# Kernel optimization log

Measured on AMD Instinct MI355X. Metric: run time of the kernel, lower is better.

## Reference

```python
import jax, jax.numpy as jnp
import numpy as np

N_NODES = 100000


def gcn_conv(x, edge_index, W, b):
    """PyG GCNConv: add self-loops, symmetric deg^{-1/2} A deg^{-1/2} aggregation.

    x: [N, Fin], edge_index: [2, E] int (row 0 = src, row 1 = dst).
    Transform first (Fin -> Fout), then gather-normalize-scatter at Fout.
    """
    n = x.shape[0]
    loops = jnp.arange(n, dtype=edge_index.dtype)
    src = jnp.concatenate([edge_index[0], loops])
    dst = jnp.concatenate([edge_index[1], loops])
    # in-degree with self-loops (all edge weights = 1)
    deg = jax.ops.segment_sum(jnp.ones_like(dst, dtype=x.dtype), dst, num_segments=n)
    dinv = jax.lax.rsqrt(deg)  # deg >= 1 thanks to self-loops
    norm = dinv[src] * dinv[dst]  # [E+N]
    h = x @ W  # [N, Fout] dense transform before sparse aggregation
    msgs = norm[:, None] * h[src]  # gather + normalize
    out = jax.ops.segment_sum(msgs, dst, num_segments=n)  # scatter-add
    return out + b


def setup_inputs() -> dict:
    key = jax.random.key(0)
    ks = jax.random.split(key, 8)
    N, E, Fin, H, C = N_NODES, 1600000, 256, 64, 11
    x = jax.random.normal(ks[0], (N, Fin), dtype=jnp.float32)
    edge_index = jax.random.randint(ks[1], (2, E), 0, N, dtype=jnp.int64)
    s1 = 1.0 / np.sqrt(Fin)
    s2 = 1.0 / np.sqrt(H)
    W1 = jax.random.uniform(ks[2], (Fin, H), jnp.float32, -s1, s1)
    b1 = jnp.zeros((H,), jnp.float32)
    W2 = jax.random.uniform(ks[3], (H, H), jnp.float32, -s2, s2)
    b2 = jnp.zeros((H,), jnp.float32)
    Wfc = jax.random.uniform(ks[4], (H, C), jnp.float32, -s2, s2)
    bfc = jax.random.uniform(ks[5], (C,), jnp.float32, -s2, s2)
    return {"x": x, "edge_index": edge_index, "W1": W1, "b1": b1,
            "W2": W2, "b2": b2, "Wfc": Wfc, "bfc": bfc}


def reference(x, edge_index, W1, b1, W2, b2, Wfc, bfc):
    h = jax.nn.relu(gcn_conv(x, edge_index, W1, b1))
    h = jax.nn.relu(gcn_conv(h, edge_index, W2, b2))
    return h @ Wfc + bfc  # [N, 11]
```

## Files before the change

kernel.cpp:

```cpp
#include <hip/hip_runtime.h>
#include <hip/hip_fp16.h>

#define NFEAT 64
#define CE 8192
#define EBUF 4608

typedef _Float16 half8 __attribute__((ext_vector_type(8)));
typedef float f32x4 __attribute__((ext_vector_type(4)));

__device__ __forceinline__ __half2 bch(unsigned int u) {
    return __builtin_bit_cast(__half2, u);
}

__global__ __launch_bounds__(256) void k_prep(
    const float* __restrict__ W1, __half* __restrict__ Wt1,
    const float* __restrict__ W2, __half* __restrict__ Wt2,
    const int* __restrict__ eiDst, int* __restrict__ hist, int E, int nbkt)
{
    __shared__ int hb[512];
    int bid = blockIdx.x, tid = threadIdx.x;
    if (bid < 64) {
        int idx = bid * 256 + tid;
        int n = idx >> 8, k = idx & 255;
        Wt1[idx] = __float2half(W1[(size_t)k * NFEAT + n]);
    } else if (bid < 80) {
        int idx = (bid - 64) * 256 + tid;
        int n = idx >> 6, k = idx & 63;
        Wt2[idx] = __float2half(W2[(size_t)k * NFEAT + n]);
    } else {
        int c = bid - 80;
        int base = c * CE;
        if (base >= E) return;
        for (int i = tid; i < nbkt; i += 256) hb[i] = 0;
        __syncthreads();
        int hi = min(base + CE, E);
        for (int e = base + tid; e < hi; e += 256)
            atomicAdd(&hb[eiDst[e] >> 8], 1);
        __syncthreads();
        for (int i = tid; i < nbkt; i += 256)
            hist[(size_t)c * nbkt + i] = hb[i];
    }
}

__global__ __launch_bounds__(256) void k_scanB(int* __restrict__ hist,
                                               int* __restrict__ cntB,
                                               int nchk, int nbkt) {
    __shared__ int hb[256];
    int b = blockIdx.x, tid = threadIdx.x;
    int v = (tid < nchk) ? hist[(size_t)tid * nbkt + b] : 0;
    hb[tid] = v;
    __syncthreads();
    for (int off = 1; off < 256; off <<= 1) {
        int t = (tid >= off) ? hb[tid - off] : 0;
        __syncthreads();
        if (tid >= off) hb[tid] += t;
        __syncthreads();
    }
    if (tid < nchk) hist[(size_t)tid * nbkt + b] = hb[tid] - v;
    if (tid == 255) cntB[b] = hb[255];
}

__global__ __launch_bounds__(256) void k_scatter(
    const int* __restrict__ ei, const int* __restrict__ hist,
    const int* __restrict__ cntB, int2* __restrict__ E2, int E, int nbkt)
{
    __shared__ int2 ebuf[CE];
    __shared__ int lofs[512];
    __shared__ int gbase[512];
    __shared__ int cur[512];
    __shared__ int hb[256];
    int c = blockIdx.x, tid = threadIdx.x;
    int base = c * CE, hi = min(base + CE, E), ne = hi - base;

    for (int i = tid; i < nbkt; i += 256) cur[i] = 0;
    __syncthreads();
    for (int e = base + tid; e < hi; e += 256)
        atomicAdd(&cur[ei[(size_t)E + e] >> 8], 1);
    __syncthreads();

    int i0 = 2 * tid, i1 = 2 * tid + 1;
    int a0 = (i0 < nbkt) ? cur[i0] : 0;
    int a1 = (i1 < nbkt) ? cur[i1] : 0;
    hb[tid] = a0 + a1;
    __syncthreads();
    for (int off = 1; off < 256; off <<= 1) {
        int t = (tid >= off) ? hb[tid - off] : 0;
        __syncthreads();
        if (tid >= off) hb[tid] += t;
        __syncthreads();
    }
    int excl = hb[tid] - (a0 + a1);
    if (i0 < nbkt) lofs[i0] = excl;
    if (i1 < nbkt) lofs[i1] = excl + a0;

    int b0 = (i0 < nbkt) ? cntB[i0] : 0;
    int b1 = (i1 < nbkt) ? cntB[i1] : 0;
    hb[tid] = b0 + b1;
    __syncthreads();
    for (int off = 1; off < 256; off <<= 1) {
        int t = (tid >= off) ? hb[tid - off] : 0;
        __syncthreads();
        if (tid >= off) hb[tid] += t;
        __syncthreads();
    }
    int excl2 = hb[tid] - (b0 + b1);
    if (i0 < nbkt) gbase[i0] = excl2 + hist[(size_t)c * nbkt + i0];
    if (i1 < nbkt) gbase[i1] = excl2 + b0 + hist[(size_t)c * nbkt + i1];

    for (int i = tid; i < nbkt; i += 256) cur[i] = lofs[i];
    __syncthreads();
    for (int e = base + tid; e < hi; e += 256) {
        int s = ei[e];
        int d = ei[(size_t)E + e];
        int p = atomicAdd(&cur[d >> 8], 1);
        ebuf[p] = make_int2(s, d);
    }
    __syncthreads();

    for (int i = tid; i < ne; i += 256) {
        int2 e = ebuf[i];
        int b = e.y >> 8;
        E2[gbase[b] + (i - lofs[b])] = e;
    }
}

__global__ __launch_bounds__(256) void k_csr(
    const int2* __restrict__ E2, const int* __restrict__ cntB,
    int* __restrict__ rowptr, float* __restrict__ dinv, int* __restrict__ col,
    int N, int E, int nbkt)
{
    __shared__ int2 ebuf[EBUF];
    __shared__ int cnt[256];
    __shared__ float dl[256];
    __shared__ int bbL[512];
    __shared__ int hb[256];
    int b = blockIdx.x, tid = threadIdx.x;

    int i0 = 2 * tid, i1 = 2 * tid + 1;
    int a0 = (i0 < nbkt) ? cntB[i0] : 0;
    int a1 = (i1 < nbkt) ? cntB[i1] : 0;
    hb[tid] = a0 + a1;
    __syncthreads();
    for (int off = 1; off < 256; off <<= 1) {
        int t = (tid >= off) ? hb[tid - off] : 0;
        __syncthreads();
        if (tid >= off) hb[tid] += t;
        __syncthreads();
    }
    int excl = hb[tid] - (a0 + a1);
    if (i0 < nbkt) bbL[i0] = excl;
    if (i1 < nbkt) bbL[i1] = excl + a0;
    __syncthreads();

    int e0 = bbL[b];
    int e1 = (b == nbkt - 1) ? E : bbL[b + 1];
    int ne = e1 - e0;
    int nL = min(ne, EBUF);

    cnt[tid] = 0;
    __syncthreads();
    for (int i = tid; i < nL; i += 256) {
        int2 e = E2[e0 + i];
        ebuf[i] = e;
        atomicAdd(&cnt[e.y & 255], 1);
    }
    for (int i = nL + tid; i < ne; i += 256) {
        int2 e = E2[e0 + i];
        atomicAdd(&cnt[e.y & 255], 1);
    }
    __syncthreads();
    int c = cnt[tid];
    dl[tid] = rsqrtf((float)(c + 1));
    for (int off = 1; off < 256; off <<= 1) {
        int t = (tid >= off) ? cnt[tid - off] : 0;
        __syncthreads();
        if (tid >= off) cnt[tid] += t;
        __syncthreads();
    }
    int texcl = cnt[tid] - c;
    int node = b * 256 + tid;
    if (node < N) {
        rowptr[node] = e0 + texcl;
        dinv[node] = dl[tid];
    }
    if (b == 0 && tid == 0) rowptr[N] = E;
    __syncthreads();
    cnt[tid] = texcl;
    __syncthreads();
    for (int i = tid; i < nL; i += 256) {
        int2 e = ebuf[i];
        int p = atomicAdd(&cnt[e.y & 255], 1);
        col[e0 + p] = e.x;
    }
    for (int i = nL + tid; i < ne; i += 256) {
        int2 e = E2[e0 + i];
        int p = atomicAdd(&cnt[e.y & 255], 1);
        col[e0 + p] = e.x;
    }
}

__global__ __launch_bounds__(256) void k_gemm1(
    const float* __restrict__ A, const __half* __restrict__ Wt,
    const float* __restrict__ dinv, __half* __restrict__ H, int M)
{
    const int K = 256;
    int tid = threadIdx.x;
    int w = tid >> 6, lane = tid & 63;
    int q = lane >> 4, n16 = lane & 15;
    int m0 = blockIdx.x * 64;

    int arow = m0 + w * 16 + n16;
    if (arow > M - 1) arow = M - 1;
    const float* ap = A + (size_t)arow * K + q * 8;
    const __half* wp = Wt + (size_t)n16 * K + q * 8;

    f32x4 acc[4];
#pragma unroll
    for (int nt = 0; nt < 4; ++nt) acc[nt] = (f32x4)(0.f);

#pragma unroll
    for (int kt = 0; kt < 8; ++kt) {
        float4 f0 = *(const float4*)(ap + kt * 32);
        float4 f1 = *(const float4*)(ap + kt * 32 + 4);
        float fv[8] = {f0.x, f0.y, f0.z, f0.w, f1.x, f1.y, f1.z, f1.w};
        half8 ahi, alo;
#pragma unroll
        for (int j = 0; j < 8; ++j) {
            _Float16 hi = (_Float16)fv[j];
            ahi[j] = hi;
            alo[j] = (_Float16)(fv[j] - (float)hi);
        }
#pragma unroll
        for (int nt = 0; nt < 4; ++nt) {
            uint4 u = *(const uint4*)(wp + (size_t)(nt * 16) * K + kt * 32);
            half8 b = __builtin_bit_cast(half8, u);
            acc[nt] = __builtin_amdgcn_mfma_f32_16x16x32_f16(ahi, b, acc[nt], 0, 0, 0);
            acc[nt] = __builtin_amdgcn_mfma_f32_16x16x32_f16(alo, b, acc[nt], 0, 0, 0);
        }
    }

#pragma unroll
    for (int reg = 0; reg < 4; ++reg) {
        int row = m0 + w * 16 + q * 4 + reg;
        if (row < M) {
            float di = dinv[row];
#pragma unroll
            for (int nt = 0; nt < 4; ++nt)
                H[(size_t)row * NFEAT + nt * 16 + n16] =
                    __float2half(di * acc[nt][reg]);
        }
    }
}

__global__ __launch_bounds__(256) void k_ag1g2(
    const __half* __restrict__ h, const int* __restrict__ rowptr,
    const int* __restrict__ col, const float* __restrict__ dinv,
    const float* __restrict__ b1, const __half* __restrict__ Wt2,
    __half* __restrict__ H2, int n)
{
    __shared__ float Bs[64][68];
    int tid = threadIdx.x;
    int w = tid >> 6, lane = tid & 63;
    int li = lane & 7, fi = li << 3;
    int slot = (w << 3) | (lane >> 3);

    const __half* hp = h + fi;
    auto ld = [&](int src) { return *(const uint4*)(hp + (size_t)src * NFEAT); };

#pragma unroll
    for (int hf = 0; hf < 2; ++hf) {
        int lr = hf * 32 + slot;
        int r = blockIdx.x * 64 + lr;
        float t0 = 0.f, t1 = 0.f, t2 = 0.f, t3 = 0.f,
              t4 = 0.f, t5 = 0.f, t6 = 0.f, t7 = 0.f;
        if (r < n) {
            float a0 = 0.f, a1 = 0.f, a2 = 0.f, a3 = 0.f,
                  a4 = 0.f, a5 = 0.f, a6 = 0.f, a7 = 0.f;
            auto addu = [&](uint4 u) {
                float2 f0 = __half22float2(bch(u.x));
                float2 f1 = __half22float2(bch(u.y));
                float2 f2 = __half22float2(bch(u.z));
                float2 f3 = __half22float2(bch(u.w));
                a0 += f0.x; a1 += f0.y; a2 += f1.x; a3 += f1.y;
                a4 += f2.x; a5 += f2.y; a6 += f3.x; a7 += f3.y;
            };
            auto p2 = [&](uint4 u0, uint4 u1) {
                uint4 s;
                s.x = __builtin_bit_cast(unsigned int, __hadd2(bch(u0.x), bch(u1.x)));
                s.y = __builtin_bit_cast(unsigned int, __hadd2(bch(u0.y), bch(u1.y)));
                s.z = __builtin_bit_cast(unsigned int, __hadd2(bch(u0.z), bch(u1.z)));
                s.w = __builtin_bit_cast(unsigned int, __hadd2(bch(u0.w), bch(u1.w)));
                addu(s);
            };
            int beg = rowptr[r], end = rowptr[r + 1];
            addu(ld(r));
            int j = beg;
            for (; j + 3 < end; j += 4) {
                uint4 u0 = ld(col[j]);
                uint4 u1 = ld(col[j + 1]);
                uint4 u2 = ld(col[j + 2]);
                uint4 u3 = ld(col[j + 3]);
                p2(u0, u1);
                p2(u2, u3);
            }
            for (; j < end; ++j) addu(ld(col[j]));
            float di = dinv[r];
            t0 = fmaxf(b1[fi + 0] + di * a0, 0.f);
            t1 = fmaxf(b1[fi + 1] + di * a1, 0.f);
            t2 = fmaxf(b1[fi + 2] + di * a2, 0.f);
            t3 = fmaxf(b1[fi + 3] + di * a3, 0.f);
            t4 = fmaxf(b1[fi + 4] + di * a4, 0.f);
            t5 = fmaxf(b1[fi + 5] + di * a5, 0.f);
            t6 = fmaxf(b1[fi + 6] + di * a6, 0.f);
            t7 = fmaxf(b1[fi + 7] + di * a7, 0.f);
        }
        *(float4*)&Bs[lr][fi]     = make_float4(t0, t1, t2, t3);
        *(float4*)&Bs[lr][fi + 4] = make_float4(t4, t5, t6, t7);
    }
    __syncthreads();

    int q = lane >> 4, n16 = lane & 15;
    f32x4 acc[4];
#pragma unroll
    for (int nt = 0; nt < 4; ++nt) acc[nt] = (f32x4)(0.f);
    const __half* wp = Wt2 + (size_t)n16 * 64 + q * 8;

#pragma unroll
    for (int kt = 0; kt < 2; ++kt) {
        const float* ap = &Bs[w * 16 + n16][kt * 32 + q * 8];
        float4 f0 = *(const float4*)ap;
        float4 f1 = *(const float4*)(ap + 4);
        float fv[8] = {f0.x, f0.y, f0.z, f0.w, f1.x, f1.y, f1.z, f1.w};
        half8 ahi, alo;
#pragma unroll
        for (int j = 0; j < 8; ++j) {
            _Float16 hi = (_Float16)fv[j];
            ahi[j] = hi;
            alo[j] = (_Float16)(fv[j] - (float)hi);
        }
#pragma unroll
        for (int nt = 0; nt < 4; ++nt) {
            uint4 u = *(const uint4*)(wp + (size_t)(nt * 16) * 64 + kt * 32);
            half8 b = __builtin_bit_cast(half8, u);
            acc[nt] = __builtin_amdgcn_mfma_f32_16x16x32_f16(ahi, b, acc[nt], 0, 0, 0);
            acc[nt] = __builtin_amdgcn_mfma_f32_16x16x32_f16(alo, b, acc[nt], 0, 0, 0);
        }
    }
#pragma unroll
    for (int reg = 0; reg < 4; ++reg) {
        int row = blockIdx.x * 64 + w * 16 + q * 4 + reg;
        if (row < n) {
            float di = dinv[row];
#pragma unroll
            for (int nt = 0; nt < 4; ++nt)
                H2[(size_t)row * NFEAT + nt * 16 + n16] =
                    __float2half(di * acc[nt][reg]);
        }
    }
}

__global__ __launch_bounds__(256) void k_aggr2(
    const __half* __restrict__ h, const int* __restrict__ rowptr,
    const int* __restrict__ col, const float* __restrict__ dinv,
    const float* __restrict__ bias, const float* __restrict__ Wfc,
    const float* __restrict__ bfc, float* __restrict__ out, int n)
{
    __shared__ float Wl[NFEAT * 11 + 11];
    int tid = threadIdx.x;
    for (int i = tid; i < NFEAT * 11; i += 256) Wl[i] = Wfc[i];
    if (tid < 11) Wl[NFEAT * 11 + tid] = bfc[tid];
    __syncthreads();

    int lane = tid & 63;
    int li = lane & 7;
    int fi = li << 3;
    int r = blockIdx.x * 32 + ((tid >> 6) << 3) + (lane >> 3);
    bool valid = r < n;

    int beg = 0, end = 0;
    if (valid) { beg = rowptr[r]; end = rowptr[r + 1]; }

    const __half* hp = h + fi;
    auto ld = [&](int src) { return *(const uint4*)(hp + (size_t)src * NFEAT); };

    float a0 = 0.f, a1 = 0.f, a2 = 0.f, a3 = 0.f,
          a4 = 0.f, a5 = 0.f, a6 = 0.f, a7 = 0.f;
    auto addu = [&](uint4 u) {
        float2 f0 = __half22float2(bch(u.x));
        float2 f1 = __half22float2(bch(u.y));
        float2 f2 = __half22float2(bch(u.z));
        float2 f3 = __half22float2(bch(u.w));
        a0 += f0.x; a1 += f0.y; a2 += f1.x; a3 += f1.y;
        a4 += f2.x; a5 += f2.y; a6 += f3.x; a7 += f3.y;
    };
    auto p2 = [&](uint4 u0, uint4 u1) {
        uint4 s;
        s.x = __builtin_bit_cast(unsigned int, __hadd2(bch(u0.x), bch(u1.x)));
        s.y = __builtin_bit_cast(unsigned int, __hadd2(bch(u0.y), bch(u1.y)));
        s.z = __builtin_bit_cast(unsigned int, __hadd2(bch(u0.z), bch(u1.z)));
        s.w = __builtin_bit_cast(unsigned int, __hadd2(bch(u0.w), bch(u1.w)));
        addu(s);
    };

    if (valid) addu(ld(r));
    int j = beg;
    for (; j + 3 < end; j += 4) {
        uint4 u0 = ld(col[j]);
        uint4 u1 = ld(col[j + 1]);
        uint4 u2 = ld(col[j + 2]);
        uint4 u3 = ld(col[j + 3]);
        p2(u0, u1);
        p2(u2, u3);
    }
    for (; j < end; ++j) addu(ld(col[j]));

    if (!valid) return;
    float di = dinv[r];
    float t0 = fmaxf(bias[fi + 0] + di * a0, 0.f);
    float t1 = fmaxf(bias[fi + 1] + di * a1, 0.f);
    float t2 = fmaxf(bias[fi + 2] + di * a2, 0.f);
    float t3 = fmaxf(bias[fi + 3] + di * a3, 0.f);
    float t4 = fmaxf(bias[fi + 4] + di * a4, 0.f);
    float t5 = fmaxf(bias[fi + 5] + di * a5, 0.f);
    float t6 = fmaxf(bias[fi + 6] + di * a6, 0.f);
    float t7 = fmaxf(bias[fi + 7] + di * a7, 0.f);

#pragma unroll
    for (int c = 0; c < 11; ++c) {
        const float* wc = &Wl[fi * 11 + c];
        float p = t0 * wc[0] + t1 * wc[11] + t2 * wc[22] + t3 * wc[33]
                + t4 * wc[44] + t5 * wc[55] + t6 * wc[66] + t7 * wc[77];
        p += __shfl_xor(p, 1, 64);
        p += __shfl_xor(p, 2, 64);
        p += __shfl_xor(p, 4, 64);
        if (li == 0) out[(size_t)r * 11 + c] = p + Wl[NFEAT * 11 + c];
    }
}

extern "C" void kernel_launch(void* const* d_in, const int* in_sizes, int n_in,
                              void* d_out, int out_size, void* d_ws, size_t ws_size,
                              hipStream_t stream) {
    const float* x   = (const float*)d_in[0];
    const int*   ei  = (const int*)d_in[1];
    const float* W1  = (const float*)d_in[2];
    const float* b1  = (const float*)d_in[3];
    const float* W2  = (const float*)d_in[4];
    const float* b2  = (const float*)d_in[5];
    const float* Wfc = (const float*)d_in[6];
    const float* bfc = (const float*)d_in[7];
    float* out = (float*)d_out;

    const int Fin = 256;
    int N = in_sizes[0] / Fin;
    int E = in_sizes[1] / 2;

    char* ws = (char*)d_ws;
    size_t off = 0;
    auto alloc = [&](size_t bytes) { void* p = ws + off; off = (off + bytes + 255) & ~(size_t)255; return p; };
    int*    rowptr = (int*)   alloc((size_t)(N + 1) * 4);
    float*  dinv   = (float*) alloc((size_t)N * 4);
    int*    col    = (int*)   alloc((size_t)E * 4);
    __half* Wt1    = (__half*)alloc((size_t)64 * 256 * 2);
    __half* Wt2    = (__half*)alloc((size_t)64 * 64 * 2);
    __half* A      = (__half*)alloc((size_t)N * NFEAT * 2);
    __half* H2     = (__half*)alloc((size_t)N * NFEAT * 2);

    int NBKT = (N + 255) >> 8;
    int NCHK = (E + CE - 1) / CE;

    int2* E2   = (int2*)alloc((size_t)E * 8);
    int*  hist = (int*) alloc((size_t)NCHK * NBKT * 4);
    int*  cntB = (int*) alloc((size_t)NBKT * 4);

    int gb = (N + 63) / 64;
    int gA = (N + 31) / 32;

    k_prep<<<80 + NCHK, 256, 0, stream>>>(W1, Wt1, W2, Wt2, ei + E, hist, E, NBKT);

    k_scanB<<<NBKT, 256, 0, stream>>>(hist, cntB, NCHK, NBKT);
    k_scatter<<<NCHK, 256, 0, stream>>>(ei, hist, cntB, E2, E, NBKT);
    k_csr<<<NBKT, 256, 0, stream>>>(E2, cntB, rowptr, dinv, col, N, E, NBKT);

    k_gemm1<<<gb, 256, 0, stream>>>(x, Wt1, dinv, A, N);

    k_ag1g2<<<gb, 256, 0, stream>>>(A, rowptr, col, dinv, b1, Wt2, H2, N);

    k_aggr2<<<gA, 256, 0, stream>>>(H2, rowptr, col, dinv, b2, Wfc, bfc, out, N);
}
```

Measured before the change: 331.9 us.

## Split GEMM1 into quarters co-scheduled with the CSR build kernels

The first dense transform no longer depends on dinv. Its 64-row tiles are split into four slices and appended as extra blocks to the histogram, scan, scatter and CSR kernels, so the tensor-core GEMM runs alongside the latency-bound graph preprocessing instead of after it. Because the source-side dinv scaling is removed from GEMM1, layer-1 aggregation now loads dinv per neighbor and uses FMA accumulation in fp32 instead of paired fp16 adds, at the cost of extra gathers. It also caches the block's rowptr slice in shared memory, and the layer-2 aggregation loop gains an 8-way unrolled stage.

After: 327.2 us. No clear change (-1.4%).

```diff
diff --git a/kernel.cpp b/kernel.cpp
--- a/kernel.cpp
+++ b/kernel.cpp
@@ -12,41 +12,111 @@
     return __builtin_bit_cast(__half2, u);
 }
 
-__global__ __launch_bounds__(256) void k_prep(
+__device__ __forceinline__ void gemm1_tile(
+    const float* __restrict__ X, const __half* __restrict__ Wt,
+    __half* __restrict__ H, int M, int tileIdx, int tid)
+{
+    const int K = 256;
+    int w = tid >> 6, lane = tid & 63;
+    int q = lane >> 4, n16 = lane & 15;
+    int m0 = tileIdx * 64;
+
+    int arow = m0 + w * 16 + n16;
+    if (arow > M - 1) arow = M - 1;
+    const float* ap = X + (size_t)arow * K + q * 8;
+    const __half* wp = Wt + (size_t)n16 * K + q * 8;
+
+    f32x4 acc[4];
+#pragma unroll
+    for (int nt = 0; nt < 4; ++nt) acc[nt] = (f32x4)(0.f);
+
+#pragma unroll
+    for (int kt = 0; kt < 8; ++kt) {
+        float4 f0 = *(const float4*)(ap + kt * 32);
+        float4 f1 = *(const float4*)(ap + kt * 32 + 4);
+        float fv[8] = {f0.x, f0.y, f0.z, f0.w, f1.x, f1.y, f1.z, f1.w};
+        half8 ahi, alo;
+#pragma unroll
+        for (int j = 0; j < 8; ++j) {
+            _Float16 hi = (_Float16)fv[j];
+            ahi[j] = hi;
+            alo[j] = (_Float16)(fv[j] - (float)hi);
+        }
+#pragma unroll
+        for (int nt = 0; nt < 4; ++nt) {
+            uint4 u = *(const uint4*)(wp + (size_t)(nt * 16) * K + kt * 32);
+            half8 b = __builtin_bit_cast(half8, u);
+            acc[nt] = __builtin_amdgcn_mfma_f32_16x16x32_f16(ahi, b, acc[nt], 0, 0, 0);
+            acc[nt] = __builtin_amdgcn_mfma_f32_16x16x32_f16(alo, b, acc[nt], 0, 0, 0);
+        }
+    }
+
+#pragma unroll
+    for (int reg = 0; reg < 4; ++reg) {
+        int row = m0 + w * 16 + q * 4 + reg;
+        if (row < M) {
+#pragma unroll
+            for (int nt = 0; nt < 4; ++nt)
+                H[(size_t)row * NFEAT + nt * 16 + n16] =
+                    __float2half(acc[nt][reg]);
+        }
+    }
+}
+
+__global__ __launch_bounds__(256) void k_cvtW(
     const float* __restrict__ W1, __half* __restrict__ Wt1,
-    const float* __restrict__ W2, __half* __restrict__ Wt2,
-    const int* __restrict__ eiDst, int* __restrict__ hist, int E, int nbkt)
-{
-    __shared__ int hb[512];
+    const float* __restrict__ W2, __half* __restrict__ Wt2)
+{
     int bid = blockIdx.x, tid = threadIdx.x;
     if (bid < 64) {
         int idx = bid * 256 + tid;
         int n = idx >> 8, k = idx & 255;
         Wt1[idx] = __float2half(W1[(size_t)k * NFEAT + n]);
-    } else if (bid < 80) {
+    } else {
         int idx = (bid - 64) * 256 + tid;
         int n = idx >> 6, k = idx & 63;
         Wt2[idx] = __float2half(W2[(size_t)k * NFEAT + n]);
-    } else {
-        int c = bid - 80;
-        int base = c * CE;
-        if (base >= E) return;
-        for (int i = tid; i < nbkt; i += 256) hb[i] = 0;
-        __syncthreads();
-        int hi = min(base + CE, E);
-        for (int e = base + tid; e < hi; e += 256)
-            atomicAdd(&hb[eiDst[e] >> 8], 1);
-        __syncthreads();
-        for (int i = tid; i < nbkt; i += 256)
-            hist[(size_t)c * nbkt + i] = hb[i];
-    }
-}
-
-__global__ __launch_bounds__(256) void k_scanB(int* __restrict__ hist,
-                                               int* __restrict__ cntB,
-                                               int nchk, int nbkt) {
+    }
+}
+
+__global__ __launch_bounds__(256) void k_hist_g(
+    const int* __restrict__ eiDst, int* __restrict__ hist, int E, int nbkt,
+    const float* __restrict__ X, const __half* __restrict__ Wt1,
+    __half* __restrict__ A, int M, int nsp, int tbase, int ntile)
+{
+    __shared__ int hb[512];
+    int bid = blockIdx.x, tid = threadIdx.x;
+    if (bid >= nsp) {
+        int t = tbase + (bid - nsp);
+        if (t < ntile) gemm1_tile(X, Wt1, A, M, t, tid);
+        return;
+    }
+    int c = bid;
+    int base = c * CE;
+    if (base >= E) return;
+    for (int i = tid; i < nbkt; i += 256) hb[i] = 0;
+    __syncthreads();
+    int hi = min(base + CE, E);
+    for (int e = base + tid; e < hi; e += 256)
+        atomicAdd(&hb[eiDst[e] >> 8], 1);
+    __syncthreads();
+    for (int i = tid; i < nbkt; i += 256)
+        hist[(size_t)c * nbkt + i] = hb[i];
+}
+
+__global__ __launch_bounds__(256) void k_scanB_g(
+    int* __restrict__ hist, int* __restrict__ cntB, int nchk, int nbkt,
+    const float* __restrict__ X, const __half* __restrict__ Wt1,
+    __half* __restrict__ A, int M, int nsp, int tbase, int ntile)
+{
     __shared__ int hb[256];
-    int b = blockIdx.x, tid = threadIdx.x;
+    int bid = blockIdx.x, tid = threadIdx.x;
+    if (bid >= nsp) {
+        int t = tbase + (bid - nsp);
+        if (t < ntile) gemm1_tile(X, Wt1, A, M, t, tid);
+        return;
+    }
+    int b = bid;
     int v = (tid < nchk) ? hist[(size_t)tid * nbkt + b] : 0;
     hb[tid] = v;
     __syncthreads();
@@ -60,16 +130,24 @@
     if (tid == 255) cntB[b] = hb[255];
 }
 
-__global__ __launch_bounds__(256) void k_scatter(
+__global__ __launch_bounds__(256) void k_scatter_g(
     const int* __restrict__ ei, const int* __restrict__ hist,
-    const int* __restrict__ cntB, int2* __restrict__ E2, int E, int nbkt)
+    const int* __restrict__ cntB, int2* __restrict__ E2, int E, int nbkt,
+    const float* __restrict__ X, const __half* __restrict__ Wt1,
+    __half* __restrict__ A, int M, int nsp, int tbase, int ntile)
 {
     __shared__ int2 ebuf[CE];
     __shared__ int lofs[512];
     __shared__ int gbase[512];
     __shared__ int cur[512];
     __shared__ int hb[256];
-    int c = blockIdx.x, tid = threadIdx.x;
+    int bid = blockIdx.x, tid = threadIdx.x;
+    if (bid >= nsp) {
+        int t = tbase + (bid - nsp);
+        if (t < ntile) gemm1_tile(X, Wt1, A, M, t, tid);
+        return;
+    }
+    int c = bid;
     int base = c * CE, hi = min(base + CE, E), ne = hi - base;
 
     for (int i = tid; i < nbkt; i += 256) cur[i] = 0;
@@ -124,17 +202,25 @@
     }
 }
 
-__global__ __launch_bounds__(256) void k_csr(
+__global__ __launch_bounds__(256) void k_csr_g(
     const int2* __restrict__ E2, const int* __restrict__ cntB,
     int* __restrict__ rowptr, float* __restrict__ dinv, int* __restrict__ col,
-    int N, int E, int nbkt)
+    int N, int E, int nbkt,
+    const float* __restrict__ X, const __half* __restrict__ Wt1,
+    __half* __restrict__ A, int M, int nsp, int tbase, int ntile)
 {
     __shared__ int2 ebuf[EBUF];
     __shared__ int cnt[256];
     __shared__ float dl[256];
     __shared__ int bbL[512];
     __shared__ int hb[256];
-    int b = blockIdx.x, tid = threadIdx.x;
+    int bid = blockIdx.x, tid = threadIdx.x;
+    if (bid >= nsp) {
+        int t = tbase + (bid - nsp);
+        if (t < ntile) gemm1_tile(X, Wt1, A, M, t, tid);
+        return;
+    }
+    int b = bid;
 
     int i0 = 2 * tid, i1 = 2 * tid + 1;
     int a0 = (i0 < nbkt) ? cntB[i0] : 0;
@@ -199,59 +285,6 @@
     }
 }
 
-__global__ __launch_bounds__(256) void k_gemm1(
-    const float* __restrict__ A, const __half* __restrict__ Wt,
-    const float* __restrict__ dinv, __half* __restrict__ H, int M)
-{
-    const int K = 256;
-    int tid = threadIdx.x;
-    int w = tid >> 6, lane = tid & 63;
-    int q = lane >> 4, n16 = lane & 15;
-    int m0 = blockIdx.x * 64;
-
-    int arow = m0 + w * 16 + n16;
-    if (arow > M - 1) arow = M - 1;
-    const float* ap = A + (size_t)arow * K + q * 8;
-    const __half* wp = Wt + (size_t)n16 * K + q * 8;
-
-    f32x4 acc[4];
-#pragma unroll
-    for (int nt = 0; nt < 4; ++nt) acc[nt] = (f32x4)(0.f);
-
-#pragma unroll
-    for (int kt = 0; kt < 8; ++kt) {
-        float4 f0 = *(const float4*)(ap + kt * 32);
-        float4 f1 = *(const float4*)(ap + kt * 32 + 4);
-        float fv[8] = {f0.x, f0.y, f0.z, f0.w, f1.x, f1.y, f1.z, f1.w};
-        half8 ahi, alo;
-#pragma unroll
-        for (int j = 0; j < 8; ++j) {
-            _Float16 hi = (_Float16)fv[j];
-            ahi[j] = hi;
-            alo[j] = (_Float16)(fv[j] - (float)hi);
-        }
-#pragma unroll
-        for (int nt = 0; nt < 4; ++nt) {
-            uint4 u = *(const uint4*)(wp + (size_t)(nt * 16) * K + kt * 32);
-            half8 b = __builtin_bit_cast(half8, u);
-            acc[nt] = __builtin_amdgcn_mfma_f32_16x16x32_f16(ahi, b, acc[nt], 0, 0, 0);
-            acc[nt] = __builtin_amdgcn_mfma_f32_16x16x32_f16(alo, b, acc[nt], 0, 0, 0);
-        }
-    }
-
-#pragma unroll
-    for (int reg = 0; reg < 4; ++reg) {
-        int row = m0 + w * 16 + q * 4 + reg;
-        if (row < M) {
-            float di = dinv[row];
-#pragma unroll
-            for (int nt = 0; nt < 4; ++nt)
-                H[(size_t)row * NFEAT + nt * 16 + n16] =
-                    __float2half(di * acc[nt][reg]);
-        }
-    }
-}
-
 __global__ __launch_bounds__(256) void k_ag1g2(
     const __half* __restrict__ h, const int* __restrict__ rowptr,
     const int* __restrict__ col, const float* __restrict__ dinv,
@@ -259,10 +292,17 @@
     __half* __restrict__ H2, int n)
 {
     __shared__ float Bs[64][68];
+    __shared__ int rpb[65];
     int tid = threadIdx.x;
     int w = tid >> 6, lane = tid & 63;
     int li = lane & 7, fi = li << 3;
     int slot = (w << 3) | (lane >> 3);
+
+    if (tid < 65) {
+        int r = blockIdx.x * 64 + tid;
+        rpb[tid] = rowptr[min(r, n)];
+    }
+    __syncthreads();
 
     const __half* hp = h + fi;
     auto ld = [&](int src) { return *(const uint4*)(hp + (size_t)src * NFEAT); };
@@ -276,35 +316,33 @@
         if (r < n) {
             float a0 = 0.f, a1 = 0.f, a2 = 0.f, a3 = 0.f,
                   a4 = 0.f, a5 = 0.f, a6 = 0.f, a7 = 0.f;
-            auto addu = [&](uint4 u) {
+            auto addus = [&](uint4 u, float dv) {
                 float2 f0 = __half22float2(bch(u.x));
                 float2 f1 = __half22float2(bch(u.y));
                 float2 f2 = __half22float2(bch(u.z));
                 float2 f3 = __half22float2(bch(u.w));
-                a0 += f0.x; a1 += f0.y; a2 += f1.x; a3 += f1.y;
-                a4 += f2.x; a5 += f2.y; a6 += f3.x; a7 += f3.y;
+                a0 = fmaf(dv, f0.x, a0); a1 = fmaf(dv, f0.y, a1);
+                a2 = fmaf(dv, f1.x, a2); a3 = fmaf(dv, f1.y, a3);
+                a4 = fmaf(dv, f2.x, a4); a5 = fmaf(dv, f2.y, a5);
+                a6 = fmaf(dv, f3.x, a6); a7 = fmaf(dv, f3.y, a7);
             };
-            auto p2 = [&](uint4 u0, uint4 u1) {
-                uint4 s;
-                s.x = __builtin_bit_cast(unsigned int, __hadd2(bch(u0.x), bch(u1.x)));
-                s.y = __builtin_bit_cast(unsigned int, __hadd2(bch(u0.y), bch(u1.y)));
-                s.z = __builtin_bit_cast(unsigned int, __hadd2(bch(u0.z), bch(u1.z)));
-                s.w = __builtin_bit_cast(unsigned int, __hadd2(bch(u0.w), bch(u1.w)));
-                addu(s);
-            };
-            int beg = rowptr[r], end = rowptr[r + 1];
-            addu(ld(r));
+            int beg = rpb[lr], end = rpb[lr + 1];
+            float di = dinv[r];
+            addus(ld(r), di);
             int j = beg;
             for (; j + 3 < end; j += 4) {
-                uint4 u0 = ld(col[j]);
-                uint4 u1 = ld(col[j + 1]);
-                uint4 u2 = ld(col[j + 2]);
-                uint4 u3 = ld(col[j + 3]);
-                p2(u0, u1);
-                p2(u2, u3);
+                int c0 = col[j], c1 = col[j + 1], c2 = col[j + 2], c3 = col[j + 3];
+                uint4 u0 = ld(c0);
+                uint4 u1 = ld(c1);
+                uint4 u2 = ld(c2);
+                uint4 u3 = ld(c3);
+                float d0 = dinv[c0], d1 = dinv[c1], d2 = dinv[c2], d3 = dinv[c3];
+                addus(u0, d0); addus(u1, d1); addus(u2, d2); addus(u3, d3);
             }
-            for (; j < end; ++j) addu(ld(col[j]));
-            float di = dinv[r];
+            for (; j < end; ++j) {
+                int cc = col[j];
+                addus(ld(cc), dinv[cc]);
+            }
             t0 = fmaxf(b1[fi + 0] + di * a0, 0.f);
             t1 = fmaxf(b1[fi + 1] + di * a1, 0.f);
             t2 = fmaxf(b1[fi + 2] + di * a2, 0.f);
@@ -404,13 +442,23 @@
 
     if (valid) addu(ld(r));
     int j = beg;
+    for (; j + 7 < end; j += 8) {
+        uint4 u0 = ld(col[j]);
+        uint4 u1 = ld(col[j + 1]);
+        uint4 u2 = ld(col[j + 2]);
+        uint4 u3 = ld(col[j + 3]);
+        uint4 u4 = ld(col[j + 4]);
+        uint4 u5 = ld(col[j + 5]);
+        uint4 u6 = ld(col[j + 6]);
+        uint4 u7 = ld(col[j + 7]);
+        p2(u0, u1); p2(u2, u3); p2(u4, u5); p2(u6, u7);
+    }
     for (; j + 3 < end; j += 4) {
         uint4 u0 = ld(col[j]);
         uint4 u1 = ld(col[j + 1]);
         uint4 u2 = ld(col[j + 2]);
         uint4 u3 = ld(col[j + 3]);
-        p2(u0, u1);
-        p2(u2, u3);
+        p2(u0, u1); p2(u2, u3);
     }
     for (; j < end; ++j) addu(ld(col[j]));
 
@@ -472,18 +520,22 @@
     int*  hist = (int*) alloc((size_t)NCHK * NBKT * 4);
     int*  cntB = (int*) alloc((size_t)NBKT * 4);
 
-    int gb = (N + 63) / 64;
+    int GT = (N + 63) / 64;
+    int GQ = (GT + 3) / 4;
     int gA = (N + 31) / 32;
 
-    k_prep<<<80 + NCHK, 256, 0, stream>>>(W1, Wt1, W2, Wt2, ei + E, hist, E, NBKT);
-
-    k_scanB<<<NBKT, 256, 0, stream>>>(hist, cntB, NCHK, NBKT);
-    k_scatter<<<NCHK, 256, 0, stream>>>(ei, hist, cntB, E2, E, NBKT);
-    k_csr<<<NBKT, 256, 0, stream>>>(E2, cntB, rowptr, dinv, col, N, E, NBKT);
-
-    k_gemm1<<<gb, 256, 0, stream>>>(x, Wt1, dinv, A, N);
-
-    k_ag1g2<<<gb, 256, 0, stream>>>(A, rowptr, col, dinv, b1, Wt2, H2, N);
+    k_cvtW<<<80, 256, 0, stream>>>(W1, Wt1, W2, Wt2);
+
+    k_hist_g<<<NCHK + GQ, 256, 0, stream>>>(
+        ei + E, hist, E, NBKT, x, Wt1, A, N, NCHK, 0, GT);
+    k_scanB_g<<<NBKT + GQ, 256, 0, stream>>>(
+        hist, cntB, NCHK, NBKT, x, Wt1, A, N, NBKT, GQ, GT);
+    k_scatter_g<<<NCHK + GQ, 256, 0, stream>>>(
+        ei, hist, cntB, E2, E, NBKT, x, Wt1, A, N, NCHK, 2 * GQ, GT);
+    k_csr_g<<<NBKT + (GT - 3 * GQ), 256, 0, stream>>>(
+        E2, cntB, rowptr, dinv, col, N, E, NBKT, x, Wt1, A, N, NBKT, 3 * GQ, GT);
+
+    k_ag1g2<<<GT, 256, 0, stream>>>(A, rowptr, col, dinv, b1, Wt2, H2, N);
 
     k_aggr2<<<gA, 256, 0, stream>>>(H2, rowptr, col, dinv, b2, Wfc, bfc, out, N);
 }
```
